# Optimization experiments

Measured on AMD Instinct MI355X. Metric: run time of the kernel, lower is better.

The kernel has to match this reference:

```python
import jax, jax.numpy as jnp
import numpy as np

V, BLOCK, L, H, E = 1000, 1024, 8, 16, 1024
D = E // H
HID = 4 * E
B, S = 4, 1024
NEG = -1e9


def setup_inputs() -> dict:
    key = jax.random.key(0)
    ks = jax.random.split(key, 10)
    s = 0.02
    rn = lambda k, shp: jax.random.normal(k, shp, jnp.float32) * s
    return dict(
        idx=jax.random.randint(ks[0], (B, S), 0, V),
        wte=rn(ks[1], (V, E)),
        wpe=rn(ks[2], (BLOCK, E)),
        ln1_w=jnp.ones((L, E), jnp.float32), ln1_b=jnp.zeros((L, E), jnp.float32),
        qkv_w=rn(ks[3], (L, E, 3 * E)), qkv_b=jnp.zeros((L, 3 * E), jnp.float32),
        out_w=rn(ks[4], (L, E, E)), out_b=jnp.zeros((L, E), jnp.float32),
        ln2_w=jnp.ones((L, E), jnp.float32), ln2_b=jnp.zeros((L, E), jnp.float32),
        fc1_w=rn(ks[5], (L, E, HID)), fc1_b=jnp.zeros((L, HID), jnp.float32),
        fc2_w=rn(ks[6], (L, HID, E)), fc2_b=jnp.zeros((L, E), jnp.float32),
        lnf_w=jnp.ones((E,), jnp.float32), lnf_b=jnp.zeros((E,), jnp.float32),
        head_w=rn(ks[7], (E, V)), head_b=jnp.zeros((V,), jnp.float32),
    )


def _ln(x, w, b):
    m = x.mean(-1, keepdims=True)
    v = x.var(-1, keepdims=True)
    return (x - m) / jnp.sqrt(v + 1e-5) * w + b


def _block(x, p):
    (ln1_w, ln1_b, qkv_w, qkv_b, out_w, out_b,
     ln2_w, ln2_b, fc1_w, fc1_b, fc2_w, fc2_b) = p
    b, s, _ = x.shape
    # --- causal self-attention ---
    h = _ln(x, ln1_w, ln1_b)
    qkv = h @ qkv_w + qkv_b                           # [b, s, 3E]
    q, k, v = jnp.split(qkv, 3, axis=-1)
    q = q.reshape(b, s, H, D)
    k = k.reshape(b, s, H, D)
    v = v.reshape(b, s, H, D)
    att = jnp.einsum('bqhd,bkhd->bhqk', q, k) / np.sqrt(D).astype(np.float32)
    mask = jnp.tril(jnp.ones((s, s), bool))
    att = jnp.where(mask, att, NEG)
    att = jax.nn.softmax(att, axis=-1)
    y = jnp.einsum('bhqk,bkhd->bqhd', att, v).reshape(b, s, E)
    x = x + (y @ out_w + out_b)
    # --- MLP ---
    h = _ln(x, ln2_w, ln2_b)
    h = jax.nn.gelu(h @ fc1_w + fc1_b, approximate=False)
    x = x + (h @ fc2_w + fc2_b)
    return x


def reference(idx, wte, wpe, ln1_w, ln1_b, qkv_w, qkv_b, out_w, out_b,
              ln2_w, ln2_b, fc1_w, fc1_b, fc2_w, fc2_b, lnf_w, lnf_b,
              head_w, head_b):
    s = idx.shape[1]
    x = wte[idx] + wpe[:s]                            # [B, S, E]
    layer_params = (ln1_w, ln1_b, qkv_w, qkv_b, out_w, out_b,
                    ln2_w, ln2_b, fc1_w, fc1_b, fc2_w, fc2_b)
    def step(x, p):
        return _block(x, p), None
    x, _ = jax.lax.scan(step, x, layer_params)
    x = _ln(x, lnf_w, lnf_b)
    logits = x @ head_w + head_b                      # [B, S, V]
    return logits
```

## Files before the change

kernel.cpp:

```cpp
#include <hip/hip_runtime.h>
#include <math.h>


typedef unsigned short u16;
typedef unsigned int u32;
typedef __attribute__((ext_vector_type(4))) float f32x4;
typedef __attribute__((ext_vector_type(8))) __bf16 bf16x8;
typedef __attribute__((ext_vector_type(8))) u16 u16x8;
typedef __attribute__((ext_vector_type(4))) u16 u16x4;

#define E 1024
#define HID 4096
#define NH 16
#define HD 64
#define SEQ 1024
#define NB 4
#define NL 8
#define MTOK 4096
#define VOC 1000

#define VMCNT(n) asm volatile("s_waitcnt vmcnt(" #n ")" ::: "memory")

__device__ __forceinline__ u16 f2bf(float f){
  u32 u = __float_as_uint(f);
  u32 r = (u + 0x7fffu + ((u >> 16) & 1u)) >> 16;
  return (u16)r;
}
__device__ __forceinline__ float bf2f(u16 b){
  return __uint_as_float((u32)b << 16);
}
__device__ __forceinline__ bf16x8 ld_bf8(const u16* p){
  return *reinterpret_cast<const bf16x8*>(p);
}
__device__ __forceinline__ bf16x8 as_bf(u16x8 v){
  return __builtin_bit_cast(bf16x8, v);
}

__device__ __forceinline__ void gload16(const void* g, void* l){
  __builtin_amdgcn_global_load_lds(
      (const __attribute__((address_space(1))) void*)g,
      (__attribute__((address_space(3))) void*)l, 16, 0, 0);
}

__global__ __launch_bounds__(256) void embed_kernel(
    const int* __restrict__ idx, const float* __restrict__ wte,
    const float* __restrict__ wpe, float* __restrict__ x)
{
  int tok = blockIdx.x, tid = threadIdx.x;
  int id = idx[tok];
  int s = tok & (SEQ - 1);
  f32x4 a = *reinterpret_cast<const f32x4*>(&wte[(size_t)id * E + tid * 4]);
  f32x4 p = *reinterpret_cast<const f32x4*>(&wpe[(size_t)s * E + tid * 4]);
  f32x4 r = a + p;
  *reinterpret_cast<f32x4*>(&x[(size_t)tok * E + tid * 4]) = r;
}

__global__ __launch_bounds__(256) void ln_kernel(
    const float* __restrict__ x, const float* __restrict__ w,
    const float* __restrict__ b, u16* __restrict__ h)
{
  int row = blockIdx.x, tid = threadIdx.x;
  const float* xr = x + (size_t)row * E;
  f32x4 v = *reinterpret_cast<const f32x4*>(xr + tid * 4);
  float s = v[0] + v[1] + v[2] + v[3];
  float q = v[0]*v[0] + v[1]*v[1] + v[2]*v[2] + v[3]*v[3];
  #pragma unroll
  for (int mm = 1; mm < 64; mm <<= 1){
    s += __shfl_xor(s, mm);
    q += __shfl_xor(q, mm);
  }
  __shared__ float red[8];
  int wv = tid >> 6;
  if ((tid & 63) == 0){ red[wv] = s; red[4 + wv] = q; }
  __syncthreads();
  s = red[0] + red[1] + red[2] + red[3];
  q = red[4] + red[5] + red[6] + red[7];
  float mean = s * (1.0f / E);
  float var = q * (1.0f / E) - mean * mean;
  float rstd = rsqrtf(var + 1e-5f);
  f32x4 wv4 = *reinterpret_cast<const f32x4*>(w + tid * 4);
  f32x4 bv4 = *reinterpret_cast<const f32x4*>(b + tid * 4);
  u16 o0 = f2bf((v[0] - mean) * rstd * wv4[0] + bv4[0]);
  u16 o1 = f2bf((v[1] - mean) * rstd * wv4[1] + bv4[1]);
  u16 o2 = f2bf((v[2] - mean) * rstd * wv4[2] + bv4[2]);
  u16 o3 = f2bf((v[3] - mean) * rstd * wv4[3] + bv4[3]);
  u16* hp = &h[(size_t)row * E + tid * 4];
  hp[0] = o0; hp[1] = o1; hp[2] = o2; hp[3] = o3;
}

__global__ __launch_bounds__(256) void wconv_kernel(
    const float* __restrict__ W, u16* __restrict__ Wt,
    int K, int Nsrc, int N)
{
  __shared__ float T[64][65];
  const int tid = threadIdx.x;
  const int n0 = blockIdx.x * 64, k0 = blockIdx.y * 64;
  const int c = (tid & 15) * 4, rbase = tid >> 4;
  if (n0 + 64 <= Nsrc){
    #pragma unroll
    for (int p = 0; p < 4; p++){
      int r = rbase + p * 16;
      f32x4 v = *reinterpret_cast<const f32x4*>(&W[(size_t)(k0 + r) * Nsrc + n0 + c]);
      T[r][c] = v[0]; T[r][c+1] = v[1]; T[r][c+2] = v[2]; T[r][c+3] = v[3];
    }
  } else {
    #pragma unroll
    for (int p = 0; p < 4; p++){
      int r = rbase + p * 16;
      #pragma unroll
      for (int j = 0; j < 4; j++){
        int n = n0 + c + j;
        T[r][c + j] = (n < Nsrc) ? W[(size_t)(k0 + r) * Nsrc + n] : 0.0f;
      }
    }
  }
  __syncthreads();
  const int nr = tid >> 2, ks = (tid & 3) * 16;
  u16x8 o0, o1;
  #pragma unroll
  for (int i = 0; i < 8; i++){
    o0[i] = f2bf(T[ks + i][nr]);
    o1[i] = f2bf(T[ks + 8 + i][nr]);
  }
  u16* dst = &Wt[(size_t)(n0 + nr) * K + k0 + ks];
  *reinterpret_cast<u16x8*>(dst) = o0;
  *reinterpret_cast<u16x8*>(dst + 8) = o1;
}

enum { EPI_BF16 = 0, EPI_GELU = 1, EPI_RESID = 2, EPI_OUT = 3 };

template<int EPI, int NW, int NWX, int FM, int FN>
__global__ __launch_bounds__(NW * 64, 2) void gemm2_kernel(
    const u16* __restrict__ A, const u16* __restrict__ Wt,
    const float* __restrict__ bias, void* __restrict__ outp,
    float* __restrict__ xres, int M, int N, int K)
{
  constexpr int BM = FM * 16 * (NW / NWX);
  constexpr int BN = FN * 16 * NWX;
  constexpr int SLOT = (BM + BN) * 32;
  extern __shared__ u16 lds[];

  const int tid = threadIdx.x;
  const int lane = tid & 63, w = tid >> 6;
  const int l15 = lane & 15, g = lane >> 4;
  const int wr = w / NWX, wc = w % NWX;
  const int wrbase = wr * FM * 16, wcbase = wc * FN * 16;

  const int nwgx = gridDim.x;
  const int bid = blockIdx.y * nwgx + blockIdx.x;
  const int cpx = (nwgx * gridDim.y) >> 3;
  const int swz = (bid & 7) * cpx + (bid >> 3);
  const int bm = (swz / nwgx) * BM, bn = (swz % nwgx) * BN;

  const u16* Abase = A + (size_t)bm * K;
  const u16* Bbase = Wt + (size_t)bn * K;

  f32x4 acc[FM][FN];
  #pragma unroll
  for (int i = 0; i < FM; i++)
    #pragma unroll
    for (int j = 0; j < FN; j++)
      acc[i][j] = f32x4{0.f, 0.f, 0.f, 0.f};

  const int lr = lane >> 2, ps = lane & 3;
  const int ss = ps ^ ((lane >> 4) & 3);
  auto STAGE = [&](int s, int cc){
    const int k0 = cc * 32;
    u16* As = lds + s * SLOT;
    u16* Bs = As + BM * 32;
    #pragma unroll
    for (int j = 0; j < 2; j++){
      int base = w * 32 + j * 16;
      gload16(&Abase[(size_t)(base + lr) * K + k0 + ss * 8], As + base * 32);
      gload16(&Bbase[(size_t)(base + lr) * K + k0 + ss * 8], Bs + base * 32);
    }
  };

  const int nt = K >> 5;
  STAGE(0, 0);
  STAGE(1, 1);
  int sl = 0;
  for (int c = 0; c < nt; c++){
    if (c + 1 < nt){ VMCNT(4); } else { VMCNT(0); }
    __builtin_amdgcn_sched_barrier(0);
    __builtin_amdgcn_s_barrier();
    __builtin_amdgcn_sched_barrier(0);

    const u16* As = lds + sl * SLOT;
    const u16* Bs = As + BM * 32;
    bf16x8 af[FM], bf[FN];
    const int rsw = (g ^ (l15 >> 2)) * 8;
    #pragma unroll
    for (int mf = 0; mf < FM; mf++)
      af[mf] = ld_bf8(&As[(wrbase + mf * 16 + l15) * 32 + rsw]);
    #pragma unroll
    for (int nf = 0; nf < FN; nf++)
      bf[nf] = ld_bf8(&Bs[(wcbase + nf * 16 + l15) * 32 + rsw]);
    __builtin_amdgcn_s_setprio(1);
    #pragma unroll
    for (int mf = 0; mf < FM; mf++)
      #pragma unroll
      for (int nf = 0; nf < FN; nf++)
        acc[mf][nf] = __builtin_amdgcn_mfma_f32_16x16x32_bf16(
            af[mf], bf[nf], acc[mf][nf], 0, 0, 0);
    __builtin_amdgcn_s_setprio(0);

    if (c + 2 < nt){
      int s2 = sl + 2; if (s2 >= 3) s2 -= 3;
      STAGE(s2, c + 2);
    }
    sl++; if (sl >= 3) sl -= 3;
  }

  #pragma unroll
  for (int mf = 0; mf < FM; mf++){
    #pragma unroll
    for (int nf = 0; nf < FN; nf++){
      int col = bn + wcbase + nf * 16 + l15;
      float bv = bias[col];
      #pragma unroll
      for (int r = 0; r < 4; r++){
        int row = bm + wrbase + mf * 16 + g * 4 + r;
        float v = acc[mf][nf][r] + bv;
        if constexpr (EPI == EPI_BF16){
          ((u16*)outp)[(size_t)row * N + col] = f2bf(v);
        } else if constexpr (EPI == EPI_GELU){
          ((u16*)outp)[(size_t)row * N + col] =
              f2bf(0.5f * v * (1.0f + erff(v * 0.70710678118654752f)));
        } else if constexpr (EPI == EPI_RESID){
          xres[(size_t)row * N + col] += v;
        } else {
          if (col < VOC)
            ((float*)outp)[(size_t)row * VOC + col] = v;
        }
      }
    }
  }
}

__global__ __launch_bounds__(512) void attn_kernel(
    const u16* __restrict__ qkv, u16* __restrict__ y)
{
  __shared__ u16 Kl[64 * 64];
  __shared__ u16 Vt[64 * 72];
  __shared__ u16 Pl[8 * 16 * 72];
  const int pr = blockIdx.x, hh = blockIdx.y, b = blockIdx.z;
  const int tid = threadIdx.x;
  const int lane = tid & 63, w = tid >> 6;
  const int l15 = lane & 15, g = lane >> 4;
  const size_t tokbase = (size_t)b * SEQ;
  const int jlo = pr, jhi = 7 - pr;
  const int qstart[2] = { jlo * 128, jhi * 128 };

  int qbase[2], dt[2];
  u16x8 q0[2], q1[2];
  f32x4 o[2][4];
  float m[2][4], llp[2][4];
  #pragma unroll
  for (int st = 0; st < 2; st++){
    qbase[st] = qstart[st] + w * 16;
    dt[st] = qbase[st] >> 6;
    const u16* qp = &qkv[(tokbase + qbase[st] + l15) * (3 * E) + hh * HD];
    u16x8 ra = *reinterpret_cast<const u16x8*>(&qp[g * 8]);
    u16x8 rb = *reinterpret_cast<const u16x8*>(&qp[32 + g * 8]);
    #pragma unroll
    for (int j = 0; j < 8; j++){
      q0[st][j] = f2bf(bf2f(ra[j]) * 0.125f);
      q1[st][j] = f2bf(bf2f(rb[j]) * 0.125f);
    }
    #pragma unroll
    for (int dc = 0; dc < 4; dc++) o[st][dc] = f32x4{0.f, 0.f, 0.f, 0.f};
    #pragma unroll
    for (int r = 0; r < 4; r++){ m[st][r] = -1e30f; llp[st][r] = 0.f; }
  }

  u16* Pw = &Pl[w * 16 * 72];
  const int T = jhi * 2 + 2;

  for (int t = 0; t < T; t++){
    const int k0 = t * 64;
    __syncthreads();
    {
      int row = w * 8 + (lane >> 3);
      int sl = lane & 7;
      const u16* src = &qkv[(tokbase + k0 + row) * (3 * E) + E + hh * HD
                            + ((sl ^ (row & 7)) * 8)];
      gload16(src, &Kl[w * 512]);
    }
    {
      int d0 = (tid & 15) * 4;
      int s  = (tid >> 4) & 15;
      int mh = tid >> 8;
      int kA = s + 32 * mh;
      const u16* vpA = &qkv[(tokbase + k0 + kA) * (3 * E) + 2 * E + hh * HD + d0];
      const u16* vpB = vpA + 16 * (3 * E);
      u16x4 va = *reinterpret_cast<const u16x4*>(vpA);
      u16x4 vb = *reinterpret_cast<const u16x4*>(vpB);
      #pragma unroll
      for (int i = 0; i < 4; i++)
        *reinterpret_cast<u32*>(&Vt[(d0 + i) * 72 + 4 * s + 2 * mh]) =
            (u32)va[i] | ((u32)vb[i] << 16);
    }
    __syncthreads();

    #pragma unroll
    for (int st = 0; st < 2; st++){
      if (t > dt[st]) continue;
      const bool diag = (t == dt[st]);
      f32x4 s[4];
      #pragma unroll
      for (int kg = 0; kg < 4; kg++){
        int key = kg * 16 + l15;
        const u16* kb = &Kl[key * 64];
        bf16x8 k0f = ld_bf8(&kb[(g ^ (key & 7)) * 8]);
        bf16x8 k1f = ld_bf8(&kb[((4 + g) ^ (key & 7)) * 8]);
        f32x4 z = f32x4{0.f, 0.f, 0.f, 0.f};
        z = __builtin_amdgcn_mfma_f32_16x16x32_bf16(as_bf(q0[st]), k0f, z, 0, 0, 0);
        z = __builtin_amdgcn_mfma_f32_16x16x32_bf16(as_bf(q1[st]), k1f, z, 0, 0, 0);
        s[kg] = z;
      }
      if (diag){
        #pragma unroll
        for (int kg = 0; kg < 4; kg++){
          int key = k0 + kg * 16 + l15;
          #pragma unroll
          for (int r = 0; r < 4; r++){
            int q = qbase[st] + g * 4 + r;
            s[kg][r] = (key <= q) ? s[kg][r] : -1e9f;
          }
        }
      }
      float lmax[4];
      bool need = false;
      #pragma unroll
      for (int r = 0; r < 4; r++){
        lmax[r] = fmaxf(fmaxf(s[0][r], s[1][r]), fmaxf(s[2][r], s[3][r]));
        need = need || (lmax[r] > m[st][r] + 8.0f);
      }
      if (__any(need)){
        #pragma unroll
        for (int r = 0; r < 4; r++){
          float x = lmax[r];
          x = fmaxf(x, __shfl_xor(x, 1));
          x = fmaxf(x, __shfl_xor(x, 2));
          x = fmaxf(x, __shfl_xor(x, 4));
          x = fmaxf(x, __shfl_xor(x, 8));
          float mn = fmaxf(m[st][r], x);
          float al = __expf(m[st][r] - mn);
          m[st][r] = mn;
          llp[st][r] *= al;
          #pragma unroll
          for (int dc = 0; dc < 4; dc++) o[st][dc][r] *= al;
        }
      }
      #pragma unroll
      for (int r = 0; r < 4; r++){
        float p0 = __expf(s[0][r] - m[st][r]);
        float p1 = __expf(s[1][r] - m[st][r]);
        float p2 = __expf(s[2][r] - m[st][r]);
        float p3 = __expf(s[3][r] - m[st][r]);
        llp[st][r] += (p0 + p1) + (p2 + p3);
        u16x4 pp = { f2bf(p0), f2bf(p1), f2bf(p2), f2bf(p3) };
        *reinterpret_cast<u16x4*>(&Pw[(g * 4 + r) * 72 + 4 * l15]) = pp;
      }
      bf16x8 pa0 = ld_bf8(&Pw[l15 * 72 + g * 8]);
      bf16x8 pa1 = ld_bf8(&Pw[l15 * 72 + 32 + g * 8]);
      #pragma unroll
      for (int dc = 0; dc < 4; dc++){
        bf16x8 v0 = ld_bf8(&Vt[(dc * 16 + l15) * 72 + g * 8]);
        bf16x8 v1 = ld_bf8(&Vt[(dc * 16 + l15) * 72 + 32 + g * 8]);
        o[st][dc] = __builtin_amdgcn_mfma_f32_16x16x32_bf16(pa0, v0, o[st][dc], 0, 0, 0);
        o[st][dc] = __builtin_amdgcn_mfma_f32_16x16x32_bf16(pa1, v1, o[st][dc], 0, 0, 0);
      }
    }
  }

  #pragma unroll
  for (int st = 0; st < 2; st++){
    #pragma unroll
    for (int r = 0; r < 4; r++){
      float rs = llp[st][r];
      rs += __shfl_xor(rs, 1);
      rs += __shfl_xor(rs, 2);
      rs += __shfl_xor(rs, 4);
      rs += __shfl_xor(rs, 8);
      float inv = 1.0f / rs;
      int row = qbase[st] + g * 4 + r;
      #pragma unroll
      for (int dc = 0; dc < 4; dc++){
        int col = hh * HD + dc * 16 + l15;
        y[(tokbase + row) * E + col] = f2bf(o[st][dc][r] * inv);
      }
    }
  }
}

__global__ __launch_bounds__(256) void biaspad_kernel(
    const float* __restrict__ hb, float* __restrict__ bpad)
{
  int i = blockIdx.x * 256 + threadIdx.x;
  if (i < 1024) bpad[i] = (i < VOC) ? hb[i] : 0.0f;
}

extern "C" void kernel_launch(void* const* d_in, const int* in_sizes, int n_in,
                              void* d_out, int out_size, void* d_ws, size_t ws_size,
                              hipStream_t stream)
{
  const int*   idx    = (const int*)  d_in[0];
  const float* wte    = (const float*)d_in[1];
  const float* wpe    = (const float*)d_in[2];
  const float* ln1_w  = (const float*)d_in[3];
  const float* ln1_b  = (const float*)d_in[4];
  const float* qkv_w  = (const float*)d_in[5];
  const float* qkv_b  = (const float*)d_in[6];
  const float* out_w  = (const float*)d_in[7];
  const float* out_b  = (const float*)d_in[8];
  const float* ln2_w  = (const float*)d_in[9];
  const float* ln2_b  = (const float*)d_in[10];
  const float* fc1_w  = (const float*)d_in[11];
  const float* fc1_b  = (const float*)d_in[12];
  const float* fc2_w  = (const float*)d_in[13];
  const float* fc2_b  = (const float*)d_in[14];
  const float* lnf_w  = (const float*)d_in[15];
  const float* lnf_b  = (const float*)d_in[16];
  const float* head_w = (const float*)d_in[17];
  const float* head_b = (const float*)d_in[18];

  char* ws = (char*)d_ws;
  float* x    = (float*)(ws + 0);
  u16*   h    = (u16*)  (ws + 16777216);
  u16*   qkvb = (u16*)  (ws + 25165824);
  u16*   y    = (u16*)  (ws + 50331648);
  u16*   g    = (u16*)  (ws + 58720256);
  u16*   wq   = (u16*)  (ws + 92274688);
  u16*   wo   = (u16*)  (ws + 98566144);
  u16*   w1   = (u16*)  (ws + 100663296);
  u16*   w2   = (u16*)  (ws + 109051904);
  u16*   wh   = (u16*)  (ws + 117440512);
  float* hbp  = (float*)(ws + 119537664);

  constexpr int LDS_BIG = 3 * (512 * 32) * 2;
  constexpr int LDS_SML = 3 * (256 * 32) * 2;
  hipFuncSetAttribute((const void*)gemm2_kernel<EPI_BF16, 8, 4, 8, 4>,
                      hipFuncAttributeMaxDynamicSharedMemorySize, LDS_BIG);
  hipFuncSetAttribute((const void*)gemm2_kernel<EPI_GELU, 8, 4, 8, 4>,
                      hipFuncAttributeMaxDynamicSharedMemorySize, LDS_BIG);

  embed_kernel<<<MTOK, 256, 0, stream>>>(idx, wte, wpe, x);
  biaspad_kernel<<<4, 256, 0, stream>>>(head_b, hbp);

  for (int l = 0; l < NL; l++){
    ln_kernel<<<MTOK, 256, 0, stream>>>(x, ln1_w + l * E, ln1_b + l * E, h);
    wconv_kernel<<<dim3(48, 16), 256, 0, stream>>>(
        qkv_w + (size_t)l * E * 3 * E, wq, E, 3 * E, 3 * E);
    gemm2_kernel<EPI_BF16, 8, 4, 8, 4><<<dim3(12, 16), 512, LDS_BIG, stream>>>(
        h, wq, qkv_b + (size_t)l * 3 * E, qkvb, nullptr, MTOK, 3 * E, E);
    attn_kernel<<<dim3(4, NH, NB), 512, 0, stream>>>(qkvb, y);
    wconv_kernel<<<dim3(16, 16), 256, 0, stream>>>(
        out_w + (size_t)l * E * E, wo, E, E, E);
    gemm2_kernel<EPI_RESID, 4, 2, 4, 4><<<dim3(8, 32), 256, LDS_SML, stream>>>(
        y, wo, out_b + (size_t)l * E, nullptr, x, MTOK, E, E);
    ln_kernel<<<MTOK, 256, 0, stream>>>(x, ln2_w + l * E, ln2_b + l * E, h);
    wconv_kernel<<<dim3(64, 16), 256, 0, stream>>>(
        fc1_w + (size_t)l * E * HID, w1, E, HID, HID);
    gemm2_kernel<EPI_GELU, 8, 4, 8, 4><<<dim3(16, 16), 512, LDS_BIG, stream>>>(
        h, w1, fc1_b + (size_t)l * HID, g, nullptr, MTOK, HID, E);
    wconv_kernel<<<dim3(16, 64), 256, 0, stream>>>(
        fc2_w + (size_t)l * HID * E, w2, HID, E, E);
    gemm2_kernel<EPI_RESID, 4, 2, 4, 4><<<dim3(8, 32), 256, LDS_SML, stream>>>(
        g, w2, fc2_b + (size_t)l * E, nullptr, x, MTOK, E, HID);
  }
  ln_kernel<<<MTOK, 256, 0, stream>>>(x, lnf_w, lnf_b, h);
  wconv_kernel<<<dim3(16, 16), 256, 0, stream>>>(head_w, wh, E, VOC, E);
  gemm2_kernel<EPI_OUT, 4, 2, 4, 4><<<dim3(8, 32), 256, LDS_SML, stream>>>(
      h, wh, hbp, (float*)d_out, nullptr, MTOK, E, E);
}
```

Baseline: 1.982 ms.

## Shrink GEMM tiles, raise occupancy hints, and halve attention block size

The big GEMMs (QKV, FC1) drop from 256x256 to 128x256 tiles with a generalized staging loop (3 row-groups per wave), which doubles grid size and allows four waves per SIMD via launch bounds. The smaller GEMMs get a min-occupancy hint of 3. The attention kernel moves to 256-thread blocks covering 64-row query chunks paired front/back, which doubles the grid. The goal is better CU fill and latency hiding, at the cost of less operand reuse per tile and tighter register budgets that may cause spills.

```diff
diff --git a/kernel.cpp b/kernel.cpp
--- a/kernel.cpp
+++ b/kernel.cpp
@@ -129,8 +129,8 @@
 
 enum { EPI_BF16 = 0, EPI_GELU = 1, EPI_RESID = 2, EPI_OUT = 3 };
 
-template<int EPI, int NW, int NWX, int FM, int FN>
-__global__ __launch_bounds__(NW * 64, 2) void gemm2_kernel(
+template<int EPI, int NW, int NWX, int FM, int FN, int MINW>
+__global__ __launch_bounds__(NW * 64, MINW) void gemm2_kernel(
     const u16* __restrict__ A, const u16* __restrict__ Wt,
     const float* __restrict__ bias, void* __restrict__ outp,
     float* __restrict__ xres, int M, int N, int K)
@@ -138,6 +138,7 @@
   constexpr int BM = FM * 16 * (NW / NWX);
   constexpr int BN = FN * 16 * NWX;
   constexpr int SLOT = (BM + BN) * 32;
+  constexpr int RPW = (BM + BN) / 16 / NW;
   extern __shared__ u16 lds[];
 
   const int tid = threadIdx.x;
@@ -169,10 +170,14 @@
     u16* As = lds + s * SLOT;
     u16* Bs = As + BM * 32;
     #pragma unroll
-    for (int j = 0; j < 2; j++){
-      int base = w * 32 + j * 16;
-      gload16(&Abase[(size_t)(base + lr) * K + k0 + ss * 8], As + base * 32);
-      gload16(&Bbase[(size_t)(base + lr) * K + k0 + ss * 8], Bs + base * 32);
+    for (int j = 0; j < RPW; j++){
+      int base = (w * RPW + j) * 16;
+      if (base < BM){
+        gload16(&Abase[(size_t)(base + lr) * K + k0 + ss * 8], As + base * 32);
+      } else {
+        int rb = base - BM;
+        gload16(&Bbase[(size_t)(rb + lr) * K + k0 + ss * 8], Bs + rb * 32);
+      }
     }
   };
 
@@ -181,7 +186,11 @@
   STAGE(1, 1);
   int sl = 0;
   for (int c = 0; c < nt; c++){
-    if (c + 1 < nt){ VMCNT(4); } else { VMCNT(0); }
+    if (c + 1 < nt){
+      if constexpr (RPW == 3) { VMCNT(3); } else { VMCNT(4); }
+    } else {
+      VMCNT(0);
+    }
     __builtin_amdgcn_sched_barrier(0);
     __builtin_amdgcn_s_barrier();
     __builtin_amdgcn_sched_barrier(0);
@@ -238,19 +247,18 @@
   }
 }
 
-__global__ __launch_bounds__(512) void attn_kernel(
+__global__ __launch_bounds__(256) void attn_kernel(
     const u16* __restrict__ qkv, u16* __restrict__ y)
 {
   __shared__ u16 Kl[64 * 64];
   __shared__ u16 Vt[64 * 72];
-  __shared__ u16 Pl[8 * 16 * 72];
+  __shared__ u16 Pl[4 * 16 * 72];
   const int pr = blockIdx.x, hh = blockIdx.y, b = blockIdx.z;
   const int tid = threadIdx.x;
   const int lane = tid & 63, w = tid >> 6;
   const int l15 = lane & 15, g = lane >> 4;
   const size_t tokbase = (size_t)b * SEQ;
-  const int jlo = pr, jhi = 7 - pr;
-  const int qstart[2] = { jlo * 128, jhi * 128 };
+  const int qstart[2] = { pr * 64, (15 - pr) * 64 };
 
   int qbase[2], dt[2];
   u16x8 q0[2], q1[2];
@@ -275,31 +283,34 @@
   }
 
   u16* Pw = &Pl[w * 16 * 72];
-  const int T = jhi * 2 + 2;
+  const int T = 16 - pr;
 
   for (int t = 0; t < T; t++){
     const int k0 = t * 64;
     __syncthreads();
-    {
-      int row = w * 8 + (lane >> 3);
+    #pragma unroll
+    for (int j = 0; j < 2; j++){
+      int row = w * 16 + j * 8 + (lane >> 3);
       int sl = lane & 7;
       const u16* src = &qkv[(tokbase + k0 + row) * (3 * E) + E + hh * HD
                             + ((sl ^ (row & 7)) * 8)];
-      gload16(src, &Kl[w * 512]);
+      gload16(src, &Kl[w * 1024 + j * 512]);
     }
     {
       int d0 = (tid & 15) * 4;
-      int s  = (tid >> 4) & 15;
-      int mh = tid >> 8;
-      int kA = s + 32 * mh;
-      const u16* vpA = &qkv[(tokbase + k0 + kA) * (3 * E) + 2 * E + hh * HD + d0];
-      const u16* vpB = vpA + 16 * (3 * E);
-      u16x4 va = *reinterpret_cast<const u16x4*>(vpA);
-      u16x4 vb = *reinterpret_cast<const u16x4*>(vpB);
-      #pragma unroll
-      for (int i = 0; i < 4; i++)
-        *reinterpret_cast<u32*>(&Vt[(d0 + i) * 72 + 4 * s + 2 * mh]) =
-            (u32)va[i] | ((u32)vb[i] << 16);
+      int s  = tid >> 4;
+      #pragma unroll
+      for (int mh = 0; mh < 2; mh++){
+        int kA = s + 32 * mh;
+        const u16* vpA = &qkv[(tokbase + k0 + kA) * (3 * E) + 2 * E + hh * HD + d0];
+        const u16* vpB = vpA + 16 * (3 * E);
+        u16x4 va = *reinterpret_cast<const u16x4*>(vpA);
+        u16x4 vb = *reinterpret_cast<const u16x4*>(vpB);
+        #pragma unroll
+        for (int i = 0; i < 4; i++)
+          *reinterpret_cast<u32*>(&Vt[(d0 + i) * 72 + 4 * s + 2 * mh]) =
+              (u32)va[i] | ((u32)vb[i] << 16);
+      }
     }
     __syncthreads();
 
@@ -439,11 +450,11 @@
   u16*   wh   = (u16*)  (ws + 117440512);
   float* hbp  = (float*)(ws + 119537664);
 
-  constexpr int LDS_BIG = 3 * (512 * 32) * 2;
+  constexpr int LDS_BIG = 3 * (384 * 32) * 2;
   constexpr int LDS_SML = 3 * (256 * 32) * 2;
-  hipFuncSetAttribute((const void*)gemm2_kernel<EPI_BF16, 8, 4, 8, 4>,
+  hipFuncSetAttribute((const void*)gemm2_kernel<EPI_BF16, 8, 4, 4, 4, 4>,
                       hipFuncAttributeMaxDynamicSharedMemorySize, LDS_BIG);
-  hipFuncSetAttribute((const void*)gemm2_kernel<EPI_GELU, 8, 4, 8, 4>,
+  hipFuncSetAttribute((const void*)gemm2_kernel<EPI_GELU, 8, 4, 4, 4, 4>,
                       hipFuncAttributeMaxDynamicSharedMemorySize, LDS_BIG);
 
   embed_kernel<<<MTOK, 256, 0, stream>>>(idx, wte, wpe, x);
@@ -453,25 +464,25 @@
     ln_kernel<<<MTOK, 256, 0, stream>>>(x, ln1_w + l * E, ln1_b + l * E, h);
     wconv_kernel<<<dim3(48, 16), 256, 0, stream>>>(
         qkv_w + (size_t)l * E * 3 * E, wq, E, 3 * E, 3 * E);
-    gemm2_kernel<EPI_BF16, 8, 4, 8, 4><<<dim3(12, 16), 512, LDS_BIG, stream>>>(
+    gemm2_kernel<EPI_BF16, 8, 4, 4, 4, 4><<<dim3(12, 32), 512, LDS_BIG, stream>>>(
         h, wq, qkv_b + (size_t)l * 3 * E, qkvb, nullptr, MTOK, 3 * E, E);
-    attn_kernel<<<dim3(4, NH, NB), 512, 0, stream>>>(qkvb, y);
+    attn_kernel<<<dim3(8, NH, NB), 256, 0, stream>>>(qkvb, y);
     wconv_kernel<<<dim3(16, 16), 256, 0, stream>>>(
         out_w + (size_t)l * E * E, wo, E, E, E);
-    gemm2_kernel<EPI_RESID, 4, 2, 4, 4><<<dim3(8, 32), 256, LDS_SML, stream>>>(
+    gemm2_kernel<EPI_RESID, 4, 2, 4, 4, 3><<<dim3(8, 32), 256, LDS_SML, stream>>>(
         y, wo, out_b + (size_t)l * E, nullptr, x, MTOK, E, E);
     ln_kernel<<<MTOK, 256, 0, stream>>>(x, ln2_w + l * E, ln2_b + l * E, h);
     wconv_kernel<<<dim3(64, 16), 256, 0, stream>>>(
         fc1_w + (size_t)l * E * HID, w1, E, HID, HID);
-    gemm2_kernel<EPI_GELU, 8, 4, 8, 4><<<dim3(16, 16), 512, LDS_BIG, stream>>>(
+    gemm2_kernel<EPI_GELU, 8, 4, 4, 4, 4><<<dim3(16, 32), 512, LDS_BIG, stream>>>(
         h, w1, fc1_b + (size_t)l * HID, g, nullptr, MTOK, HID, E);
     wconv_kernel<<<dim3(16, 64), 256, 0, stream>>>(
         fc2_w + (size_t)l * HID * E, w2, HID, E, E);
-    gemm2_kernel<EPI_RESID, 4, 2, 4, 4><<<dim3(8, 32), 256, LDS_SML, stream>>>(
+    gemm2_kernel<EPI_RESID, 4, 2, 4, 4, 3><<<dim3(8, 32), 256, LDS_SML, stream>>>(
         g, w2, fc2_b + (size_t)l * E, nullptr, x, MTOK, E, HID);
   }
   ln_kernel<<<MTOK, 256, 0, stream>>>(x, lnf_w, lnf_b, h);
   wconv_kernel<<<dim3(16, 16), 256, 0, stream>>>(head_w, wh, E, VOC, E);
-  gemm2_kernel<EPI_OUT, 4, 2, 4, 4><<<dim3(8, 32), 256, LDS_SML, stream>>>(
+  gemm2_kernel<EPI_OUT, 4, 2, 4, 4, 3><<<dim3(8, 32), 256, LDS_SML, stream>>>(
       h, wh, hbp, (float*)d_out, nullptr, MTOK, E, E);
 }
```

Result: no change. 2.003 ms (+1.1%).
